# Performance work log

Hardware: AMD Instinct MI355X
Metric: run time of the kernel (lower is better)

The kernel has to match this reference:

```python
import jax, jax.numpy as jnp
import numpy as np

EPS = 1e-5

def _conv_bn_relu(x, w, gamma, beta):
    # x: [B, C, N], w: [O, C] (1x1 conv, no bias)
    y = jnp.einsum('oc,bcn->bon', w, x)
    # BatchNorm1d in training mode: per-channel stats over (B, N)
    mean = jnp.mean(y, axis=(0, 2), keepdims=True)
    var = jnp.var(y, axis=(0, 2), keepdims=True)
    yhat = (y - mean) * jax.lax.rsqrt(var + EPS)
    return jax.nn.relu(gamma[None, :, None] * yhat + beta[None, :, None])


def setup_inputs() -> dict:
    key = jax.random.key(0)
    ks = jax.random.split(key, 8)
    B, C, N, Cr = 4, 256, 4096, 32
    x = jax.random.normal(ks[0], (B, C, N), dtype=jnp.float32)
    w1 = jax.random.normal(ks[1], (Cr, C), dtype=jnp.float32) * (1.0 / np.sqrt(C))
    w2 = jax.random.normal(ks[2], (Cr, C), dtype=jnp.float32) * (1.0 / np.sqrt(C))
    w3 = jax.random.normal(ks[3], (C, C), dtype=jnp.float32) * (1.0 / np.sqrt(C))
    g1 = 1.0 + 0.1 * jax.random.normal(ks[4], (Cr,), dtype=jnp.float32)
    b1 = 0.1 * jax.random.normal(ks[5], (Cr,), dtype=jnp.float32)
    g2 = 1.0 + 0.1 * jax.random.normal(ks[6], (Cr,), dtype=jnp.float32)
    b2 = 0.1 * jax.random.normal(ks[7], (Cr,), dtype=jnp.float32)
    g3 = jnp.ones((C,), dtype=jnp.float32)
    b3 = jnp.zeros((C,), dtype=jnp.float32)
    return {'x': x, 'w1': w1, 'w2': w2, 'w3': w3,
            'g1': g1, 'b1': b1, 'g2': g2, 'b2': b2, 'g3': g3, 'b3': b3}


def reference(x, w1, w2, w3, g1, b1, g2, b2, g3, b3):
    # a: [B, N, Cr] (queries), k: [B, Cr, N] (keys)
    a = _conv_bn_relu(x, w1, g1, b1).transpose(0, 2, 1)
    k = _conv_bn_relu(x, w2, g2, b2)
    # s[b, n, m] = softmax_m(sum_c a[b,n,c] * k[b,c,m])
    s = jax.nn.softmax(jnp.einsum('bnc,bcm->bnm', a, k), axis=-1)
    d = _conv_bn_relu(x, w3, g3, b3)  # [B, C, N]
    # out = x + d @ s^T : out[b,c,m] = sum_n d[b,c,n] * s[m,n]
    out = x + jnp.einsum('bcn,bmn->bcm', d, s)
    return out
```

## Files before the change

### kernel.cpp

```cpp
#include <hip/hip_runtime.h>
#include <cstddef>
#include <cstdint>

#define B_ 4
#define C_ 256
#define N_ 4096
#define KF_OFF_B  ((size_t)1024 * 1024)
#define DF_OFF_B  ((size_t)2 * 1024 * 1024)
#define SUM_OFF_B ((size_t)10 * 1024 * 1024)
#define ML_OFF_B  (SUM_OFF_B + 1280 * 4)
#define XH_OFF_B  (ML_OFF_B + 524288)
#define XL_OFF_B  (XH_OFF_B + (size_t)8 * 1024 * 1024)
#define WH_OFF_B  (XL_OFF_B + (size_t)8 * 1024 * 1024)
#define WL_OFF_B  (WH_OFF_B + 163840)
#define LOG2E 1.4426950408889634f

typedef unsigned short bfraw;
typedef __attribute__((ext_vector_type(8))) short short8;
typedef __attribute__((ext_vector_type(4))) float float4v;
typedef __attribute__((ext_vector_type(4))) bfraw bfraw4;

__device__ inline bfraw f2bf(float f) {
    union { float f; uint32_t u; } c; c.f = f;
    uint32_t u = c.u;
    u += 0x7fffu + ((u >> 16) & 1u);
    return (bfraw)(u >> 16);
}
__device__ inline float bf2f(bfraw h) {
    union { uint32_t u; float f; } c; c.u = ((uint32_t)h) << 16;
    return c.f;
}
#if __has_builtin(__builtin_amdgcn_exp2f)
__device__ inline float EXP2(float x) { return __builtin_amdgcn_exp2f(x); }
#else
__device__ inline float EXP2(float x) { return exp2f(x); }
#endif
__device__ inline uint32_t pack2(float a, float b) {
    union { float f; uint32_t u; } ca, cb; ca.f = a; cb.f = b;
#if __has_builtin(__builtin_amdgcn_perm)
    return __builtin_amdgcn_perm(cb.u + 0x8000u, ca.u + 0x8000u, 0x07060302u);
#else
    return ((ca.u + 0x8000u) >> 16) | ((cb.u + 0x8000u) & 0xffff0000u);
#endif
}

__global__ __launch_bounds__(256) void prep_kernel(
    const float* __restrict__ x,
    const float* __restrict__ w1, const float* __restrict__ w2,
    const float* __restrict__ w3, uint8_t* __restrict__ wsb)
{
    __shared__ float Ls[64][65];
    if (blockIdx.x >= 1024) {
        int bid = blockIdx.x - 1024;
        if (bid == 0) {
            float* sums = (float*)(wsb + SUM_OFF_B);
            for (int i = threadIdx.x; i < 640; i += 256) sums[i] = 0.f;
        }
        bfraw* wh = (bfraw*)(wsb + WH_OFF_B);
        bfraw* wl = (bfraw*)(wsb + WL_OFF_B);
        int idx4 = (bid * 256 + threadIdx.x) * 4;
        int ch = idx4 >> 8, k = idx4 & 255;
        const float* wr = (ch < 32) ? (w1 + ch * C_)
                          : (ch < 64) ? (w2 + (ch - 32) * C_)
                                      : (w3 + (ch - 64) * C_);
        float4 v = *(const float4*)&wr[k];
        float va[4] = {v.x, v.y, v.z, v.w};
        bfraw4 h, l;
#pragma unroll
        for (int j = 0; j < 4; ++j) {
            h[j] = f2bf(va[j]);
            l[j] = f2bf(va[j] - bf2f(h[j]));
        }
        *(bfraw4*)&wh[idx4] = h;
        *(bfraw4*)&wl[idx4] = l;
        return;
    }
    bfraw* xh = (bfraw*)(wsb + XH_OFF_B);
    bfraw* xl = (bfraw*)(wsb + XL_OFF_B);
    const int id = blockIdx.x;
    const int b  = id >> 8;
    const int c0 = ((id >> 6) & 3) << 6;
    const int n0 = (id & 63) << 6;
    const int t  = threadIdx.x;
    {
        int cl = t >> 4, nc = (t & 15) << 2;
#pragma unroll
        for (int i = 0; i < 4; ++i) {
            float4 v = *(const float4*)&x[((size_t)b * C_ + c0 + cl + i * 16) * N_ + n0 + nc];
            Ls[cl + i * 16][nc + 0] = v.x;
            Ls[cl + i * 16][nc + 1] = v.y;
            Ls[cl + i * 16][nc + 2] = v.z;
            Ls[cl + i * 16][nc + 3] = v.w;
        }
    }
    __syncthreads();
    int nl = t >> 2, seg = t & 3;
    bfraw hb[16], lb[16];
#pragma unroll
    for (int j = 0; j < 16; ++j) {
        float v = Ls[seg * 16 + j][nl];
        bfraw h = f2bf(v);
        hb[j] = h;
        lb[j] = f2bf(v - bf2f(h));
    }
    size_t base = ((size_t)b * N_ + n0 + nl) * 256 + c0 + seg * 16;
    *(short8*)&xh[base]     = *(short8*)&hb[0];
    *(short8*)&xh[base + 8] = *(short8*)&hb[8];
    *(short8*)&xl[base]     = *(short8*)&lb[0];
    *(short8*)&xl[base + 8] = *(short8*)&lb[8];
}

__global__ __launch_bounds__(256, 2) void ygemm_kernel(uint8_t* __restrict__ wsb)
{
    const bfraw* xh = (const bfraw*)(wsb + XH_OFF_B);
    const bfraw* xl = (const bfraw*)(wsb + XL_OFF_B);
    const bfraw* wh = (const bfraw*)(wsb + WH_OFF_B);
    const bfraw* wl = (const bfraw*)(wsb + WL_OFF_B);
    bfraw* qf  = (bfraw*)wsb;
    bfraw* kfp = (bfraw*)(wsb + KF_OFF_B);
    bfraw* dfp = (bfraw*)(wsb + DF_OFF_B);
    float* sums  = (float*)(wsb + SUM_OFF_B);
    float* sumsq = sums + 320;
    __shared__ float redS[4][64], redQ[4][64];

    const int bx = blockIdx.x;
    const int by = blockIdx.y;
    const int b  = bx >> 5;
    const int n0 = (bx << 7) & (N_ - 1);
    const int t = threadIdx.x, w = t >> 6, l = t & 63, lq = l & 15, lg = l >> 4;
    const int nw = n0 + w * 32;

    float4v acc[4][2];
#pragma unroll
    for (int i = 0; i < 4; ++i)
#pragma unroll
        for (int j = 0; j < 2; ++j) acc[i][j] = (float4v){0.f, 0.f, 0.f, 0.f};

    for (int s = 0; s < 8; ++s) {
        const int k0 = s * 32;
        short8 ah[4], al[4], bh[2], bl[2];
#pragma unroll
        for (int ct = 0; ct < 4; ++ct) {
            size_t off = (size_t)(by * 64 + ct * 16 + lq) * 256 + k0 + lg * 8;
            ah[ct] = *(const short8*)&wh[off];
            al[ct] = *(const short8*)&wl[off];
        }
#pragma unroll
        for (int nt = 0; nt < 2; ++nt) {
            size_t off = ((size_t)b * N_ + nw + nt * 16 + lq) * 256 + k0 + lg * 8;
            bh[nt] = *(const short8*)&xh[off];
            bl[nt] = *(const short8*)&xl[off];
        }
#pragma unroll
        for (int ct = 0; ct < 4; ++ct)
#pragma unroll
            for (int nt = 0; nt < 2; ++nt) {
                acc[ct][nt] = __builtin_amdgcn_mfma_f32_16x16x32_bf16(ah[ct], bh[nt], acc[ct][nt], 0, 0, 0);
                acc[ct][nt] = __builtin_amdgcn_mfma_f32_16x16x32_bf16(al[ct], bh[nt], acc[ct][nt], 0, 0, 0);
                acc[ct][nt] = __builtin_amdgcn_mfma_f32_16x16x32_bf16(ah[ct], bl[nt], acc[ct][nt], 0, 0, 0);
            }
    }
#pragma unroll
    for (int ct = 0; ct < 4; ++ct) {
        float sv[4], qv[4];
#pragma unroll
        for (int r = 0; r < 4; ++r) {
            float a0 = acc[ct][0][r], a1 = acc[ct][1][r];
            sv[r] = a0 + a1;
            qv[r] = a0 * a0 + a1 * a1;
#pragma unroll
            for (int m = 1; m < 16; m <<= 1) {
                sv[r] += __shfl_xor(sv[r], m);
                qv[r] += __shfl_xor(qv[r], m);
            }
        }
        if (lq == 0) {
#pragma unroll
            for (int r = 0; r < 4; ++r) {
                redS[w][ct * 16 + lg * 4 + r] = sv[r];
                redQ[w][ct * 16 + lg * 4 + r] = qv[r];
            }
        }
    }
    __syncthreads();
    if (t < 64) {
        float s = redS[0][t] + redS[1][t] + redS[2][t] + redS[3][t];
        float q = redQ[0][t] + redQ[1][t] + redQ[2][t] + redQ[3][t];
        atomicAdd(&sums[by * 64 + t], s);
        atomicAdd(&sumsq[by * 64 + t], q);
    }
    if (by == 0) {
#pragma unroll
        for (int ct = 0; ct < 4; ++ct)
#pragma unroll
            for (int nt = 0; nt < 2; ++nt)
#pragma unroll
                for (int r = 0; r < 4; ++r) {
                    int c = ct * 16 + lg * 4 + r;
                    int n = nw + nt * 16 + lq;
                    size_t addr = ((size_t)(b << 8) + (n >> 4)) * 512
                                + (size_t)(((n & 15) | (((c >> 3) & 3) << 4)) << 3) + (c & 7);
                    bfraw v = f2bf(acc[ct][nt][r]);
                    if (c < 32) qf[addr] = v; else kfp[addr] = v;
                }
    } else {
#pragma unroll
        for (int ct = 0; ct < 4; ++ct)
#pragma unroll
            for (int nt = 0; nt < 2; ++nt)
#pragma unroll
                for (int r = 0; r < 4; ++r) {
                    int cg = (by - 1) * 64 + ct * 16 + lg * 4 + r;
                    int n = nw + nt * 16 + lq;
                    size_t addr = (((size_t)(b << 4) + (cg >> 4)) * 128 + (n >> 5)) * 512
                                + (size_t)(((cg & 15) | (((n >> 3) & 3) << 4)) << 3) + (n & 7);
                    dfp[addr] = f2bf(acc[ct][nt][r]);
                }
    }
}

__device__ inline void bn_coef(const float* __restrict__ sums,
                               const float* __restrict__ g1, const float* __restrict__ b1,
                               const float* __restrict__ g2, const float* __restrict__ b2,
                               const float* __restrict__ g3, const float* __restrict__ b3,
                               int ch, float& sc, float& bi)
{
    const float inv = 1.0f / (float)(B_ * N_);
    float mean = sums[ch] * inv;
    float var  = sums[320 + ch] * inv - mean * mean;
    float g, bb;
    if (ch < 32)      { g = g1[ch];      bb = b1[ch]; }
    else if (ch < 64) { g = g2[ch - 32]; bb = b2[ch - 32]; }
    else              { g = g3[ch - 64]; bb = b3[ch - 64]; }
    sc = g * rsqrtf(var + 1e-5f);
    bi = bb - sc * mean;
    if (ch < 32) { sc *= LOG2E; bi *= LOG2E; }
}

__global__ __launch_bounds__(256) void affine_kernel(
    uint8_t* __restrict__ wsb,
    const float* __restrict__ g1, const float* __restrict__ b1,
    const float* __restrict__ g2, const float* __restrict__ b2,
    const float* __restrict__ g3, const float* __restrict__ b3)
{
    bfraw* base = (bfraw*)wsb;
    const float* sums = (const float*)(wsb + SUM_OFF_B);
    size_t i8 = ((size_t)blockIdx.x * 256 + threadIdx.x) * 8;
    bfraw4 v0 = *(bfraw4*)&base[i8];
    bfraw4 v1 = *(bfraw4*)&base[i8 + 4];
    if (i8 < 1048576) {
        int ch0 = (((int)(i8 >> 7)) & 3) * 8 + ((i8 < 524288) ? 0 : 32);
        float sa[8], ca[8];
#pragma unroll
        for (int j = 0; j < 8; ++j)
            bn_coef(sums, g1, b1, g2, b2, g3, b3, ch0 + j, sa[j], ca[j]);
#pragma unroll
        for (int j = 0; j < 4; ++j) {
            v0[j] = f2bf(fmaxf(0.f, fmaf(sa[j],     bf2f(v0[j]), ca[j])));
            v1[j] = f2bf(fmaxf(0.f, fmaf(sa[j + 4], bf2f(v1[j]), ca[j + 4])));
        }
    } else {
        size_t rel = i8 - 1048576;
        int ch = 64 + (((int)(rel >> 16)) & 15) * 16 + (((int)(rel >> 3)) & 15);
        float s, b;
        bn_coef(sums, g1, b1, g2, b2, g3, b3, ch, s, b);
#pragma unroll
        for (int j = 0; j < 4; ++j) {
            v0[j] = f2bf(fmaxf(0.f, fmaf(s, bf2f(v0[j]), b)));
            v1[j] = f2bf(fmaxf(0.f, fmaf(s, bf2f(v1[j]), b)));
        }
    }
    *(bfraw4*)&base[i8] = v0;
    *(bfraw4*)&base[i8 + 4] = v1;
}

__global__ __launch_bounds__(512, 2) void flash_kernel(
    const float* __restrict__ x, const uint8_t* __restrict__ wsb,
    float* __restrict__ out)
{
    const bfraw* qf  = (const bfraw*)wsb;
    const bfraw* kfp = (const bfraw*)(wsb + KF_OFF_B);
    const bfraw* dfp = (const bfraw*)(wsb + DF_OFF_B);
    __shared__ bfraw Pl[2][64 * 256];
    __shared__ bfraw kst[2][16 * 512];
    __shared__ float lsh[2][64];

    const int id  = blockIdx.x;
    const int b   = id & 3;
    const int n0q = (id >> 2) << 6;
    const int tid = threadIdx.x;
    const int w   = tid >> 6;
    const int l   = tid & 63;
    const int lq  = l & 15;
    const int lg  = l >> 4;
    const int sw  = lq & 7;
    const int qt_s   = w >> 1;
    const int ks_loc = w & 1;
    const int qp  = w >> 2;
    const int cq  = w & 3;

    const short8 qfrag = *(const short8*)&qf[((size_t)(b * 256 + (n0q >> 4) + qt_s)) * 512 + l * 8];
    const float4v zv = {-16.f, -16.f, -16.f, -16.f};

    float ps = 0.f;
    float4v acc[4][2];
#pragma unroll
    for (int i = 0; i < 4; ++i)
#pragma unroll
        for (int j = 0; j < 2; ++j) acc[i][j] = (float4v){0.f, 0.f, 0.f, 0.f};

    short8 dfr[4][4];
#pragma unroll
    for (int i = 0; i < 4; ++i)
#pragma unroll
        for (int c = 0; c < 4; ++c)
            dfr[i][c] = *(const short8*)&dfp[(((size_t)(b * 16 + cq + 4 * i)) * 128 + c) * 512 + l * 8];
    {
        short8 v0 = *(const short8*)&kfp[((size_t)(b * 256 + w)) * 512 + l * 8];
        short8 v1 = *(const short8*)&kfp[((size_t)(b * 256 + w + 8)) * 512 + l * 8];
        *(short8*)&kst[0][w * 512 + l * 8] = v0;
        *(short8*)&kst[0][(w + 8) * 512 + l * 8] = v1;
    }
    __syncthreads();

    const int qrow = qt_s * 16 + lq;
    for (int it = 0; it < 16; ++it) {
        const int ib = it & 1;
        const int nit = (it + 1) & 15;
        short8 kstage0 = *(const short8*)&kfp[((size_t)(b * 256 + nit * 16 + w)) * 512 + l * 8];
        short8 kstage1 = *(const short8*)&kfp[((size_t)(b * 256 + nit * 16 + w + 8)) * 512 + l * 8];
        short8 kfr[8];
#pragma unroll
        for (int kt = 0; kt < 8; ++kt)
            kfr[kt] = *(const short8*)&kst[ib][(ks_loc * 8 + kt) * 512 + l * 8];
        float4v st[8];
#pragma unroll
        for (int kt = 0; kt < 8; ++kt)
            st[kt] = __builtin_amdgcn_mfma_f32_16x16x32_bf16(kfr[kt], qfrag, zv, 0, 0, 0);
#pragma unroll
        for (int kt = 0; kt < 8; ++kt) {
            float e0 = EXP2(st[kt][0]);
            float e1 = EXP2(st[kt][1]);
            float e2 = EXP2(st[kt][2]);
            float e3 = EXP2(st[kt][3]);
            ps += (e0 + e1) + (e2 + e3);
            uint2 pd = {pack2(e0, e1), pack2(e2, e3)};
            int g = (2 * (ks_loc * 8 + kt) + (lg >> 1)) ^ sw;
            *(uint2*)&Pl[ib][qrow * 256 + g * 8 + (lg & 1) * 4] = pd;
        }
        *(short8*)&kst[ib ^ 1][w * 512 + l * 8] = kstage0;
        *(short8*)&kst[ib ^ 1][(w + 8) * 512 + l * 8] = kstage1;
        __syncthreads();
#pragma unroll
        for (int ch = 0; ch < 8; ++ch) {
            short8 bfr[2];
            int g = (ch * 4 + lg) ^ sw;
#pragma unroll
            for (int qt = 0; qt < 2; ++qt)
                bfr[qt] = *(const short8*)&Pl[ib][((2 * qp + qt) * 16 + lq) * 256 + g * 8];
            __builtin_amdgcn_s_setprio(1);
#pragma unroll
            for (int i = 0; i < 4; ++i)
#pragma unroll
                for (int qt = 0; qt < 2; ++qt)
                    acc[i][qt] = __builtin_amdgcn_mfma_f32_16x16x32_bf16(dfr[i][ch & 3], bfr[qt], acc[i][qt], 0, 0, 0);
            __builtin_amdgcn_s_setprio(0);
            int rch = (ch < 4) ? (it * 8 + ch + 4) : (nit * 8 + ch - 4);
#pragma unroll
            for (int i = 0; i < 4; ++i)
                dfr[i][ch & 3] = *(const short8*)&dfp[(((size_t)(b * 16 + cq + 4 * i)) * 128 + rch) * 512 + l * 8];
        }
    }
    ps += __shfl_xor(ps, 16);
    ps += __shfl_xor(ps, 32);
    if (lg == 0) lsh[ks_loc][qrow] = ps;
    __syncthreads();
    float inv[2];
#pragma unroll
    for (int qt = 0; qt < 2; ++qt) {
        int qg = (2 * qp + qt) * 16 + lq;
        inv[qt] = 1.0f / (lsh[0][qg] + lsh[1][qg]);
    }
#pragma unroll
    for (int i = 0; i < 4; ++i) {
        int ctg = cq + 4 * i;
#pragma unroll
        for (int r = 0; r < 4; ++r) {
            int c = ctg * 16 + lg * 4 + r;
            size_t base = ((size_t)b * C_ + c) * N_ + n0q;
#pragma unroll
            for (int qt = 0; qt < 2; ++qt) {
                size_t idx = base + (2 * qp + qt) * 16 + lq;
                out[idx] = x[idx] + acc[i][qt][r] * inv[qt];
            }
        }
    }
}

extern "C" void kernel_launch(void* const* d_in, const int* in_sizes, int n_in,
                              void* d_out, int out_size, void* d_ws, size_t ws_size,
                              hipStream_t stream) {
    (void)in_sizes; (void)n_in; (void)out_size; (void)ws_size;
    const float* x  = (const float*)d_in[0];
    const float* w1 = (const float*)d_in[1];
    const float* w2 = (const float*)d_in[2];
    const float* w3 = (const float*)d_in[3];
    const float* g1 = (const float*)d_in[4];
    const float* b1 = (const float*)d_in[5];
    const float* g2 = (const float*)d_in[6];
    const float* b2 = (const float*)d_in[7];
    const float* g3 = (const float*)d_in[8];
    const float* b3 = (const float*)d_in[9];
    uint8_t* wsb = (uint8_t*)d_ws;
    float* outp = (float*)d_out;

    prep_kernel<<<1104, 256, 0, stream>>>(x, w1, w2, w3, wsb);
    ygemm_kernel<<<dim3(128, 5), 256, 0, stream>>>(wsb);
    affine_kernel<<<2560, 256, 0, stream>>>(wsb, g1, b1, g2, b2, g3, b3);
    flash_kernel<<<256, 512, 0, stream>>>(x, wsb, outp);
}
```

Before: 184.2 us.

## Vectorize projection stores via LDS transpose and remap PV wave tiling

The ygemm epilogue now writes the q/k fragments as 4-wide bf16 vectors. The d projection is staged through a per-wave LDS tile so it can be written to global memory as contiguous 16-byte stores instead of scattered 2-byte stores. In the attention kernel each wave now owns 2 channel tiles across all 4 query tiles, instead of 4 channel tiles across 2 query tiles. It keeps the full 8-chunk d fragments in registers and prefetches the next iteration's chunks, which raises LDS P-fragment reads per wave but simplifies the d prefetch indexing. The change adds LDS use and a barrier in ygemm and may shift register pressure.

```diff
diff --git a/kernel.cpp b/kernel.cpp
--- a/kernel.cpp
+++ b/kernel.cpp
@@ -122,6 +122,7 @@
     float* sums  = (float*)(wsb + SUM_OFF_B);
     float* sumsq = sums + 320;
     __shared__ float redS[4][64], redQ[4][64];
+    __shared__ bfraw Td[4][64 * 40];
 
     const int bx = blockIdx.x;
     const int by = blockIdx.y;
@@ -193,29 +194,36 @@
 #pragma unroll
         for (int ct = 0; ct < 4; ++ct)
 #pragma unroll
+            for (int nt = 0; nt < 2; ++nt) {
+                int n = nw + nt * 16 + lq;
+                int c0 = ct * 16 + lg * 4;
+                bfraw4 v;
+#pragma unroll
+                for (int r = 0; r < 4; ++r) v[r] = f2bf(acc[ct][nt][r]);
+                size_t addr = ((size_t)(b << 8) + (n >> 4)) * 512
+                            + (size_t)(((n & 15) | (((c0 >> 3) & 3) << 4)) << 3) + (c0 & 7);
+                if (c0 < 32) *(bfraw4*)&qf[addr] = v;
+                else         *(bfraw4*)&kfp[addr] = v;
+            }
+    } else {
+#pragma unroll
+        for (int ct = 0; ct < 4; ++ct)
+#pragma unroll
             for (int nt = 0; nt < 2; ++nt)
 #pragma unroll
                 for (int r = 0; r < 4; ++r) {
-                    int c = ct * 16 + lg * 4 + r;
-                    int n = nw + nt * 16 + lq;
-                    size_t addr = ((size_t)(b << 8) + (n >> 4)) * 512
-                                + (size_t)(((n & 15) | (((c >> 3) & 3) << 4)) << 3) + (c & 7);
-                    bfraw v = f2bf(acc[ct][nt][r]);
-                    if (c < 32) qf[addr] = v; else kfp[addr] = v;
+                    int cl = ct * 16 + lg * 4 + r;
+                    int nl = nt * 16 + lq;
+                    Td[w][cl * 40 + nl] = f2bf(acc[ct][nt][r]);
                 }
-    } else {
-#pragma unroll
-        for (int ct = 0; ct < 4; ++ct)
-#pragma unroll
-            for (int nt = 0; nt < 2; ++nt)
-#pragma unroll
-                for (int r = 0; r < 4; ++r) {
-                    int cg = (by - 1) * 64 + ct * 16 + lg * 4 + r;
-                    int n = nw + nt * 16 + lq;
-                    size_t addr = (((size_t)(b << 4) + (cg >> 4)) * 128 + (n >> 5)) * 512
-                                + (size_t)(((cg & 15) | (((n >> 3) & 3) << 4)) << 3) + (n & 7);
-                    dfp[addr] = f2bf(acc[ct][nt][r]);
-                }
+        __syncthreads();
+#pragma unroll
+        for (int ctl = 0; ctl < 4; ++ctl) {
+            short8 vv = *(const short8*)&Td[w][(ctl * 16 + (l & 15)) * 40 + (l >> 4) * 8];
+            size_t addr = (((size_t)(b << 4) + (by - 1) * 4 + ctl) * 128 + (nw >> 5)) * 512
+                        + (size_t)l * 8;
+            *(short8*)&dfp[addr] = vv;
+        }
     }
 }
 
@@ -296,25 +304,25 @@
     const int sw  = lq & 7;
     const int qt_s   = w >> 1;
     const int ks_loc = w & 1;
-    const int qp  = w >> 2;
-    const int cq  = w & 3;
+    const int ctg0 = w;
+    const int ctg1 = 8 + w;
 
     const short8 qfrag = *(const short8*)&qf[((size_t)(b * 256 + (n0q >> 4) + qt_s)) * 512 + l * 8];
     const float4v zv = {-16.f, -16.f, -16.f, -16.f};
 
     float ps = 0.f;
-    float4v acc[4][2];
-#pragma unroll
-    for (int i = 0; i < 4; ++i)
-#pragma unroll
-        for (int j = 0; j < 2; ++j) acc[i][j] = (float4v){0.f, 0.f, 0.f, 0.f};
-
-    short8 dfr[4][4];
-#pragma unroll
-    for (int i = 0; i < 4; ++i)
-#pragma unroll
-        for (int c = 0; c < 4; ++c)
-            dfr[i][c] = *(const short8*)&dfp[(((size_t)(b * 16 + cq + 4 * i)) * 128 + c) * 512 + l * 8];
+    float4v acc[2][4];
+#pragma unroll
+    for (int i = 0; i < 2; ++i)
+#pragma unroll
+        for (int j = 0; j < 4; ++j) acc[i][j] = (float4v){0.f, 0.f, 0.f, 0.f};
+
+    short8 dfr[2][8];
+#pragma unroll
+    for (int ch = 0; ch < 8; ++ch) {
+        dfr[0][ch] = *(const short8*)&dfp[(((size_t)(b * 16 + ctg0)) * 128 + ch) * 512 + l * 8];
+        dfr[1][ch] = *(const short8*)&dfp[(((size_t)(b * 16 + ctg1)) * 128 + ch) * 512 + l * 8];
+    }
     {
         short8 v0 = *(const short8*)&kfp[((size_t)(b * 256 + w)) * 512 + l * 8];
         short8 v1 = *(const short8*)&kfp[((size_t)(b * 256 + w + 8)) * 512 + l * 8];
@@ -353,45 +361,43 @@
         __syncthreads();
 #pragma unroll
         for (int ch = 0; ch < 8; ++ch) {
-            short8 bfr[2];
+            short8 bfr[4];
             int g = (ch * 4 + lg) ^ sw;
 #pragma unroll
-            for (int qt = 0; qt < 2; ++qt)
-                bfr[qt] = *(const short8*)&Pl[ib][((2 * qp + qt) * 16 + lq) * 256 + g * 8];
+            for (int qt = 0; qt < 4; ++qt)
+                bfr[qt] = *(const short8*)&Pl[ib][(qt * 16 + lq) * 256 + g * 8];
             __builtin_amdgcn_s_setprio(1);
 #pragma unroll
-            for (int i = 0; i < 4; ++i)
-#pragma unroll
-                for (int qt = 0; qt < 2; ++qt)
-                    acc[i][qt] = __builtin_amdgcn_mfma_f32_16x16x32_bf16(dfr[i][ch & 3], bfr[qt], acc[i][qt], 0, 0, 0);
+            for (int qt = 0; qt < 4; ++qt) {
+                acc[0][qt] = __builtin_amdgcn_mfma_f32_16x16x32_bf16(dfr[0][ch], bfr[qt], acc[0][qt], 0, 0, 0);
+                acc[1][qt] = __builtin_amdgcn_mfma_f32_16x16x32_bf16(dfr[1][ch], bfr[qt], acc[1][qt], 0, 0, 0);
+            }
             __builtin_amdgcn_s_setprio(0);
-            int rch = (ch < 4) ? (it * 8 + ch + 4) : (nit * 8 + ch - 4);
-#pragma unroll
-            for (int i = 0; i < 4; ++i)
-                dfr[i][ch & 3] = *(const short8*)&dfp[(((size_t)(b * 16 + cq + 4 * i)) * 128 + rch) * 512 + l * 8];
+            dfr[0][ch] = *(const short8*)&dfp[(((size_t)(b * 16 + ctg0)) * 128 + nit * 8 + ch) * 512 + l * 8];
+            dfr[1][ch] = *(const short8*)&dfp[(((size_t)(b * 16 + ctg1)) * 128 + nit * 8 + ch) * 512 + l * 8];
         }
     }
     ps += __shfl_xor(ps, 16);
     ps += __shfl_xor(ps, 32);
     if (lg == 0) lsh[ks_loc][qrow] = ps;
     __syncthreads();
-    float inv[2];
-#pragma unroll
-    for (int qt = 0; qt < 2; ++qt) {
-        int qg = (2 * qp + qt) * 16 + lq;
+    float inv[4];
+#pragma unroll
+    for (int qt = 0; qt < 4; ++qt) {
+        int qg = qt * 16 + lq;
         inv[qt] = 1.0f / (lsh[0][qg] + lsh[1][qg]);
     }
 #pragma unroll
-    for (int i = 0; i < 4; ++i) {
-        int ctg = cq + 4 * i;
+    for (int ct = 0; ct < 2; ++ct) {
+        int ctg = ct ? ctg1 : ctg0;
 #pragma unroll
         for (int r = 0; r < 4; ++r) {
             int c = ctg * 16 + lg * 4 + r;
             size_t base = ((size_t)b * C_ + c) * N_ + n0q;
 #pragma unroll
-            for (int qt = 0; qt < 2; ++qt) {
-                size_t idx = base + (2 * qp + qt) * 16 + lq;
-                out[idx] = x[idx] + acc[i][qt][r] * inv[qt];
+            for (int qt = 0; qt < 4; ++qt) {
+                size_t idx = base + qt * 16 + lq;
+                out[idx] = x[idx] + acc[ct][qt][r] * inv[qt];
             }
         }
     }
```

New measurement: 172.8 us. -6.2%, faster.
